# Kernel tuning notes

Hardware: AMD Instinct MI355X
Metric: run time of the kernel (lower is better)

Reference implementation:

```python
import jax, jax.numpy as jnp
import numpy as np

B, S, D = 2, 2048, 1024
H, HD = 16, 64  # num_heads, head_dim; H*HD == D


def setup_inputs() -> dict:
    key = jax.random.key(0)
    ks = jax.random.split(key, 5)
    scale = 1.0 / np.sqrt(D)
    return {
        "inputs": jax.random.normal(ks[0], (B, S, D), jnp.float32),
        "Wq": jax.random.normal(ks[1], (D, H * HD), jnp.float32) * scale,
        "bq": jnp.zeros((H * HD,), jnp.float32),
        "Wk": jax.random.normal(ks[2], (D, H * HD), jnp.float32) * scale,
        "bk": jnp.zeros((H * HD,), jnp.float32),
        "Wv": jax.random.normal(ks[3], (D, H * HD), jnp.float32) * scale,
        "bv": jnp.zeros((H * HD,), jnp.float32),
        "Wo": jax.random.normal(ks[4], (H * HD, D), jnp.float32) * scale,
        "bo": jnp.zeros((D,), jnp.float32),
    }


def reference(inputs, Wq, bq, Wk, bk, Wv, bv, Wo, bo):
    b, s, _ = inputs.shape
    # QKV projections, split into heads: [b, s, H, HD]
    q = (inputs @ Wq + bq).reshape(b, s, H, HD)
    k = (inputs @ Wk + bk).reshape(b, s, H, HD)
    v = (inputs @ Wv + bv).reshape(b, s, H, HD)
    # scaled dot-product attention (non-causal, full)
    scores = jnp.einsum('bqhd,bkhd->bhqk', q, k) / jnp.sqrt(jnp.float32(HD))
    attn = jax.nn.softmax(scores, axis=-1)
    out = jnp.einsum('bhql,blhd->bqhd', attn, v).reshape(b, s, H * HD)
    return out @ Wo + bo
```

## Files before the change

kernel.cpp:

```cpp
#include <hip/hip_runtime.h>
#include <hip/hip_bf16.h>

typedef __attribute__((ext_vector_type(8))) _Float16 half8;
typedef __attribute__((ext_vector_type(4))) _Float16 half4;
typedef __attribute__((ext_vector_type(2))) _Float16 half2v;
typedef __attribute__((ext_vector_type(4))) __fp16 fp16x4;
typedef __attribute__((ext_vector_type(4))) float f32x4;

#define MFMA16(a, b, c) __builtin_amdgcn_mfma_f32_16x16x32_f16(a, b, c, 0, 0, 0)
#define MFMA16K16(a, b, c)                                                         \
    __builtin_amdgcn_mfma_f32_16x16x16f16(__builtin_bit_cast(fp16x4, a),           \
                                          __builtin_bit_cast(fp16x4, b), c, 0, 0, 0)

typedef const __attribute__((address_space(1))) unsigned int GU32;
typedef __attribute__((address_space(3))) unsigned int LU32;

__device__ __forceinline__ void async_copy16(const _Float16* g, _Float16* l) {
    __builtin_amdgcn_global_load_lds((GU32*)g, (LU32*)l, 16, 0, 0);
}

__device__ __forceinline__ half2v pack2(float a, float b) {
    return __builtin_bit_cast(half2v, __builtin_amdgcn_cvt_pkrtz(a, b));
}

#define QSCALE 0.18033688011112042f

__global__ __launch_bounds__(256) void prep(
    const float* __restrict__ X, _Float16* __restrict__ Xh,
    const float* __restrict__ W0, const float* __restrict__ W1,
    const float* __restrict__ W2, const float* __restrict__ W3,
    _Float16* __restrict__ T0, _Float16* __restrict__ T1,
    _Float16* __restrict__ T2, _Float16* __restrict__ T3) {
    __shared__ float t[32][33];
    const int bid = blockIdx.x, tid = threadIdx.x;
    if (bid < 4096) {
        int i = (bid * 256 + tid) * 4;
        float4 v = *(const float4*)(X + i);
        half4 o = {(_Float16)v.x, (_Float16)v.y, (_Float16)v.z, (_Float16)v.w};
        *(half4*)(Xh + i) = o;
    } else {
        const int bid2 = bid - 4096;
        const int z = bid2 >> 10, tt = bid2 & 1023;
        const int bx = tt & 31, by = tt >> 5;
        const int tx = tid & 31, ty = tid >> 5;
        const float* src = z == 0 ? W0 : z == 1 ? W1 : z == 2 ? W2 : W3;
        _Float16* dst    = z == 0 ? T0 : z == 1 ? T1 : z == 2 ? T2 : T3;
        const int x = bx * 32 + tx;
        const int y0 = by * 32;
        for (int i = ty; i < 32; i += 8)
            t[i][tx] = src[(size_t)(y0 + i) * 1024 + x];
        __syncthreads();
        const int nx = y0 + tx;
        const int ny = bx * 32;
        for (int i = ty; i < 32; i += 8)
            dst[(size_t)(ny + i) * 1024 + nx] = (_Float16)t[tx][i];
    }
}

__global__ __launch_bounds__(256) void qkv_gemm(
    const _Float16* __restrict__ Xh,
    const _Float16* __restrict__ WTq, const _Float16* __restrict__ WTk,
    const _Float16* __restrict__ WTv,
    const float* __restrict__ bq, const float* __restrict__ bk,
    const float* __restrict__ bv,
    _Float16* __restrict__ Qo, _Float16* __restrict__ Ko,
    _Float16* __restrict__ Vto) {
    __shared__ __attribute__((aligned(16))) _Float16 Als[128 * 32];
    __shared__ __attribute__((aligned(16))) _Float16 Bls[128 * 32];

    const int wsel = blockIdx.y >> 3;
    const _Float16* WT = wsel == 0 ? WTq : wsel == 1 ? WTk : WTv;
    const float* bias  = wsel == 0 ? bq  : wsel == 1 ? bk  : bv;

    const int tid = threadIdx.x, w = tid >> 6, lane = tid & 63;
    const int quad = lane >> 4, l16 = lane & 15;
    const int wr = (w >> 1) * 64, wc = (w & 1) * 64;
    const int mBase = blockIdx.x * 128, nBase = (blockIdx.y & 7) * 128;
    const _Float16* Ab = Xh + (size_t)mBase * 1024;
    const _Float16* Bb = WT + (size_t)nBase * 1024;

    f32x4 acc[4][4] = {};

    for (int k0 = 0; k0 < 1024; k0 += 32) {
        __syncthreads();
#pragma unroll
        for (int iss = 0; iss < 2; ++iss) {
            int u = iss * 256 + tid;
            int r = u >> 2, c8 = (u & 3) * 8;
            _Float16* lA = Als + (size_t)(iss * 256 + (tid & 192)) * 8;
            _Float16* lB = Bls + (size_t)(iss * 256 + (tid & 192)) * 8;
            async_copy16(Ab + (size_t)r * 1024 + k0 + c8, lA);
            async_copy16(Bb + (size_t)r * 1024 + k0 + c8, lB);
        }
        __syncthreads();
        half8 af[4], bfr[4];
#pragma unroll
        for (int i = 0; i < 4; ++i) af[i]  = ((const half8*)Als)[(wr + i * 16 + l16) * 4 + quad];
#pragma unroll
        for (int j = 0; j < 4; ++j) bfr[j] = ((const half8*)Bls)[(wc + j * 16 + l16) * 4 + quad];
#pragma unroll
        for (int i = 0; i < 4; ++i)
#pragma unroll
            for (int j = 0; j < 4; ++j) acc[i][j] = MFMA16(af[i], bfr[j], acc[i][j]);
    }

    const float scale = (wsel == 0) ? QSCALE : 1.0f;
#pragma unroll
    for (int i = 0; i < 4; ++i) {
        const int row = mBase + wr + i * 16 + quad * 4;
#pragma unroll
        for (int j = 0; j < 4; ++j) {
            const int col = nBase + wc + j * 16 + l16;
            const float bb = bias[col];
            const int hh = col >> 6, hd = col & 63;
            if (wsel == 2) {
                const int bi = row >> 11, s = row & 2047;
                half4 pv;
#pragma unroll
                for (int r = 0; r < 4; ++r) pv[r] = (_Float16)((acc[i][j][r] + bb) * scale);
                *(half4*)(Vto + ((size_t)(bi * 16 + hh) * 64 + hd) * 2048 + s) = pv;
            } else {
                _Float16* dst = (wsel == 0) ? Qo : Ko;
#pragma unroll
                for (int r = 0; r < 4; ++r) {
                    const int token = row + r;
                    const int bi = token >> 11, s = token & 2047;
                    dst[((size_t)(bi * 16 + hh) * 2048 + s) * 64 + hd] =
                        (_Float16)((acc[i][j][r] + bb) * scale);
                }
            }
        }
    }
}

__global__ __launch_bounds__(512) void attn_kernel(
    const _Float16* __restrict__ Q, const _Float16* __restrict__ K,
    const _Float16* __restrict__ Vt, _Float16* __restrict__ O) {
    const int bh = blockIdx.y;
    const int b = bh >> 4, h = bh & 15;
    const int qt = blockIdx.x;
    const int tid = threadIdx.x, w = tid >> 6, lane = tid & 63;
    const int quad = lane >> 4, l16 = lane & 15;
    const int ws2 = w & 3, stream = w >> 2;

    __shared__ __attribute__((aligned(16))) _Float16 smem[32768];
    _Float16 (*Kls)[2][4096] = (_Float16(*)[2][4096])smem;
    _Float16 (*Vls)[2][4096] = (_Float16(*)[2][4096])(smem + 16384);

    const _Float16* Qb = Q  + (size_t)bh * 2048 * 64;
    const _Float16* Kb = K  + (size_t)bh * 2048 * 64;
    const _Float16* Vb = Vt + (size_t)bh * 64 * 2048;

    const int stid = tid & 255, sgrp = tid >> 8;
    const int u0 = stid, u1 = 256 + stid;
    const int r0 = u0 >> 3, c0 = (u0 & 7) ^ (r0 & 7);
    const int r1 = u1 >> 3, c1 = (u1 & 7) ^ (r1 & 7);
    const int lbase0 = (stid & 192) * 8;
    const int lbase1 = 2048 + (stid & 192) * 8;

    half8 qf[2][2];
#pragma unroll
    for (int g = 0; g < 2; ++g) {
        const int q = qt * 128 + ws2 * 32 + g * 16 + l16;
#pragma unroll
        for (int kc = 0; kc < 2; ++kc)
            qf[g][kc] = *(const half8*)(Qb + (size_t)q * 64 + kc * 32 + quad * 8);
    }

    f32x4 oacc[2][4] = {};
    float l[2] = {0.f, 0.f};

    {
        const int nb = sgrp * 64;
        _Float16* kd = &Kls[sgrp][0][0];
        _Float16* vd = &Vls[sgrp][0][0];
        async_copy16(Kb + (size_t)(nb + r0) * 64 + c0 * 8, kd + lbase0);
        async_copy16(Kb + (size_t)(nb + r1) * 64 + c1 * 8, kd + lbase1);
        async_copy16(Vb + (size_t)r0 * 2048 + nb + c0 * 8, vd + lbase0);
        async_copy16(Vb + (size_t)r1 * 2048 + nb + c1 * 8, vd + lbase1);
    }

    const int sw = l16 & 7;
    for (int it = 0; it < 16; ++it) {
        __syncthreads();
        const _Float16* Kc = &Kls[stream][it & 1][0];
        const _Float16* Vc = &Vls[stream][it & 1][0];
        if (it + 1 < 16) {
            const int nb = (2 * (it + 1) + sgrp) * 64;
            _Float16* kd = &Kls[sgrp][(it + 1) & 1][0];
            _Float16* vd = &Vls[sgrp][(it + 1) & 1][0];
            async_copy16(Kb + (size_t)(nb + r0) * 64 + c0 * 8, kd + lbase0);
            async_copy16(Kb + (size_t)(nb + r1) * 64 + c1 * 8, kd + lbase1);
            async_copy16(Vb + (size_t)r0 * 2048 + nb + c0 * 8, vd + lbase0);
            async_copy16(Vb + (size_t)r1 * 2048 + nb + c1 * 8, vd + lbase1);
        }
        f32x4 s0[4] = {}, s1[4] = {};
#pragma unroll
        for (int nt = 0; nt < 4; ++nt) {
            const int key = nt * 16 + l16;
            half8 k0 = *(const half8*)(Kc + ((size_t)key * 8 + (quad ^ sw)) * 8);
            half8 k1 = *(const half8*)(Kc + ((size_t)key * 8 + ((4 + quad) ^ sw)) * 8);
            s0[nt] = MFMA16(k0, qf[0][0], s0[nt]);
            s0[nt] = MFMA16(k1, qf[0][1], s0[nt]);
            s1[nt] = MFMA16(k0, qf[1][0], s1[nt]);
            s1[nt] = MFMA16(k1, qf[1][1], s1[nt]);
        }
        half4 pB[2][4];
#pragma unroll
        for (int g = 0; g < 2; ++g) {
            f32x4* s = g ? s1 : s0;
#pragma unroll
            for (int nt = 0; nt < 4; ++nt) {
                float p0 = __builtin_amdgcn_exp2f(s[nt][0]);
                float p1 = __builtin_amdgcn_exp2f(s[nt][1]);
                float p2 = __builtin_amdgcn_exp2f(s[nt][2]);
                float p3 = __builtin_amdgcn_exp2f(s[nt][3]);
                l[g] += (p0 + p1) + (p2 + p3);
                ((half2v*)&pB[g][nt])[0] = pack2(p0, p1);
                ((half2v*)&pB[g][nt])[1] = pack2(p2, p3);
            }
        }
#pragma unroll
        for (int nt = 0; nt < 4; ++nt) {
            const int chunk = (nt << 1) + (quad >> 1);
#pragma unroll
            for (int j = 0; j < 4; ++j) {
                const int hd = j * 16 + l16;
                half4 vf = *(const half4*)(Vc + ((size_t)hd * 8 + (chunk ^ sw)) * 8 +
                                           (quad & 1) * 4);
                oacc[0][j] = MFMA16K16(vf, pB[0][nt], oacc[0][j]);
                oacc[1][j] = MFMA16K16(vf, pB[1][nt], oacc[1][j]);
            }
        }
    }
    __syncthreads();
    float* red  = (float*)smem;
    float* redl = (float*)smem + 4 * 64 * 36;
    const int rb = (ws2 * 64 + lane) * 36;
    if (stream == 1) {
#pragma unroll
        for (int g = 0; g < 2; ++g) {
#pragma unroll
            for (int j = 0; j < 4; ++j)
                *(f32x4*)&red[rb + (g * 4 + j) * 4] = oacc[g][j];
            redl[(ws2 * 64 + lane) * 2 + g] = l[g];
        }
    }
    __syncthreads();
    if (stream == 0) {
#pragma unroll
        for (int g = 0; g < 2; ++g) {
#pragma unroll
            for (int j = 0; j < 4; ++j) {
                f32x4 o2 = *(const f32x4*)&red[rb + (g * 4 + j) * 4];
#pragma unroll
                for (int r = 0; r < 4; ++r) oacc[g][j][r] += o2[r];
            }
            float lt = l[g] + redl[(ws2 * 64 + lane) * 2 + g];
            lt += __shfl_xor(lt, 16);
            lt += __shfl_xor(lt, 32);
            const float inv = __builtin_amdgcn_rcpf(lt);
            const int token = b * 2048 + qt * 128 + ws2 * 32 + g * 16 + l16;
#pragma unroll
            for (int j = 0; j < 4; ++j) {
                half4 ov;
#pragma unroll
                for (int r = 0; r < 4; ++r) ov[r] = (_Float16)(oacc[g][j][r] * inv);
                *(half4*)&O[(size_t)token * 1024 + h * 64 + j * 16 + quad * 4] = ov;
            }
        }
    }
}

__global__ __launch_bounds__(256) void out_gemm(
    const _Float16* __restrict__ Oh, const _Float16* __restrict__ WTo,
    const float* __restrict__ bo, float* __restrict__ Y) {
    __shared__ __attribute__((aligned(16))) _Float16 Als[64 * 32];
    __shared__ __attribute__((aligned(16))) _Float16 Bls[128 * 32];
    const int tid = threadIdx.x, w = tid >> 6, lane = tid & 63;
    const int quad = lane >> 4, l16 = lane & 15;
    const int wr = (w >> 1) * 32, wc = (w & 1) * 64;
    const int mBase = blockIdx.x * 64, nBase = blockIdx.y * 128;
    const _Float16* Ab = Oh + (size_t)mBase * 1024;
    const _Float16* Bb = WTo + (size_t)nBase * 1024;

    f32x4 acc[2][4] = {};
    for (int k0 = 0; k0 < 1024; k0 += 32) {
        __syncthreads();
        {
            int r = tid >> 2, c8 = (tid & 3) * 8;
            _Float16* lA = Als + (size_t)(tid & 192) * 8;
            async_copy16(Ab + (size_t)r * 1024 + k0 + c8, lA);
        }
#pragma unroll
        for (int iss = 0; iss < 2; ++iss) {
            int u = iss * 256 + tid;
            int r = u >> 2, c8 = (u & 3) * 8;
            _Float16* lB = Bls + (size_t)(iss * 256 + (tid & 192)) * 8;
            async_copy16(Bb + (size_t)r * 1024 + k0 + c8, lB);
        }
        __syncthreads();
        half8 af[2], bfr[4];
#pragma unroll
        for (int i = 0; i < 2; ++i) af[i]  = ((const half8*)Als)[(wr + i * 16 + l16) * 4 + quad];
#pragma unroll
        for (int j = 0; j < 4; ++j) bfr[j] = ((const half8*)Bls)[(wc + j * 16 + l16) * 4 + quad];
#pragma unroll
        for (int i = 0; i < 2; ++i)
#pragma unroll
            for (int j = 0; j < 4; ++j) acc[i][j] = MFMA16(af[i], bfr[j], acc[i][j]);
    }
#pragma unroll
    for (int i = 0; i < 2; ++i) {
        const int row = mBase + wr + i * 16 + quad * 4;
#pragma unroll
        for (int j = 0; j < 4; ++j) {
            const int col = nBase + wc + j * 16 + l16;
            const float bb = bo[col];
#pragma unroll
            for (int r = 0; r < 4; ++r)
                Y[(size_t)(row + r) * 1024 + col] = acc[i][j][r] + bb;
        }
    }
}

extern "C" void kernel_launch(void* const* d_in, const int* in_sizes, int n_in,
                              void* d_out, int out_size, void* d_ws, size_t ws_size,
                              hipStream_t stream) {
    const float* X  = (const float*)d_in[0];
    const float* Wq = (const float*)d_in[1];
    const float* bq = (const float*)d_in[2];
    const float* Wk = (const float*)d_in[3];
    const float* bk = (const float*)d_in[4];
    const float* Wv = (const float*)d_in[5];
    const float* bv = (const float*)d_in[6];
    const float* Wo = (const float*)d_in[7];
    const float* bo = (const float*)d_in[8];
    float* Y = (float*)d_out;

    char* ws = (char*)d_ws;
    _Float16* Xh  = (_Float16*)(ws);
    _Float16* WTq = (_Float16*)(ws + (8ull << 20));
    _Float16* WTk = (_Float16*)(ws + (10ull << 20));
    _Float16* WTv = (_Float16*)(ws + (12ull << 20));
    _Float16* WTo = (_Float16*)(ws + (14ull << 20));
    _Float16* Qh  = (_Float16*)(ws + (16ull << 20));
    _Float16* Kh  = (_Float16*)(ws + (24ull << 20));
    _Float16* Vth = (_Float16*)(ws + (32ull << 20));
    _Float16* Oh  = (_Float16*)(ws + (40ull << 20));

    prep<<<8192, 256, 0, stream>>>(X, Xh, Wq, Wk, Wv, Wo, WTq, WTk, WTv, WTo);
    qkv_gemm<<<dim3(32, 24), 256, 0, stream>>>(Xh, WTq, WTk, WTv, bq, bk, bv, Qh, Kh, Vth);
    attn_kernel<<<dim3(16, 32), 512, 0, stream>>>(Qh, Kh, Vth, Oh);
    out_gemm<<<dim3(64, 8), 256, 0, stream>>>(Oh, WTo, bo, Y);
}
```

Measured before the change: 200.5 us.

## Swizzle GEMM LDS tiles and store Q/K token-major to simplify epilogue

Both projection GEMMs now XOR-swizzle the 16-byte chunk position within each LDS row, on the global load side and the fragment read side, to cut LDS bank conflicts on the MFMA operand reads. Q and K are also written token-major ([b, s, h*64]) with contiguous column stores instead of a per-head scattered layout. The attention kernel indexes Q and K with a 1024 stride to match. This trades a simpler, more coalesced QKV epilogue for strided 128-byte row reads of K and Q in attention.

```diff
diff --git a/kernel.cpp b/kernel.cpp
--- a/kernel.cpp
+++ b/kernel.cpp
@@ -24,6 +24,7 @@
 }
 
 #define QSCALE 0.18033688011112042f
+
 
 __global__ __launch_bounds__(256) void prep(
     const float* __restrict__ X, _Float16* __restrict__ Xh,
@@ -79,25 +80,35 @@
     const _Float16* Ab = Xh + (size_t)mBase * 1024;
     const _Float16* Bb = WT + (size_t)nBase * 1024;
 
+    const int sr0 = tid >> 2,          sc0 = (tid & 3) ^ ((sr0 >> 1) & 3);
+    const int sr1 = (256 + tid) >> 2,  sc1 = (tid & 3) ^ ((sr1 >> 1) & 3);
+
     f32x4 acc[4][4] = {};
 
     for (int k0 = 0; k0 < 1024; k0 += 32) {
         __syncthreads();
-#pragma unroll
-        for (int iss = 0; iss < 2; ++iss) {
-            int u = iss * 256 + tid;
-            int r = u >> 2, c8 = (u & 3) * 8;
-            _Float16* lA = Als + (size_t)(iss * 256 + (tid & 192)) * 8;
-            _Float16* lB = Bls + (size_t)(iss * 256 + (tid & 192)) * 8;
-            async_copy16(Ab + (size_t)r * 1024 + k0 + c8, lA);
-            async_copy16(Bb + (size_t)r * 1024 + k0 + c8, lB);
+        {
+            _Float16* lA0 = Als + (size_t)(tid & 192) * 8;
+            _Float16* lB0 = Bls + (size_t)(tid & 192) * 8;
+            _Float16* lA1 = Als + (size_t)(256 + (tid & 192)) * 8;
+            _Float16* lB1 = Bls + (size_t)(256 + (tid & 192)) * 8;
+            async_copy16(Ab + (size_t)sr0 * 1024 + k0 + sc0 * 8, lA0);
+            async_copy16(Bb + (size_t)sr0 * 1024 + k0 + sc0 * 8, lB0);
+            async_copy16(Ab + (size_t)sr1 * 1024 + k0 + sc1 * 8, lA1);
+            async_copy16(Bb + (size_t)sr1 * 1024 + k0 + sc1 * 8, lB1);
         }
         __syncthreads();
         half8 af[4], bfr[4];
 #pragma unroll
-        for (int i = 0; i < 4; ++i) af[i]  = ((const half8*)Als)[(wr + i * 16 + l16) * 4 + quad];
-#pragma unroll
-        for (int j = 0; j < 4; ++j) bfr[j] = ((const half8*)Bls)[(wc + j * 16 + l16) * 4 + quad];
+        for (int i = 0; i < 4; ++i) {
+            const int row = wr + i * 16 + l16;
+            af[i] = ((const half8*)Als)[row * 4 + (quad ^ ((row >> 1) & 3))];
+        }
+#pragma unroll
+        for (int j = 0; j < 4; ++j) {
+            const int row = wc + j * 16 + l16;
+            bfr[j] = ((const half8*)Bls)[row * 4 + (quad ^ ((row >> 1) & 3))];
+        }
 #pragma unroll
         for (int i = 0; i < 4; ++i)
 #pragma unroll
@@ -112,8 +123,8 @@
         for (int j = 0; j < 4; ++j) {
             const int col = nBase + wc + j * 16 + l16;
             const float bb = bias[col];
-            const int hh = col >> 6, hd = col & 63;
             if (wsel == 2) {
+                const int hh = col >> 6, hd = col & 63;
                 const int bi = row >> 11, s = row & 2047;
                 half4 pv;
 #pragma unroll
@@ -122,12 +133,9 @@
             } else {
                 _Float16* dst = (wsel == 0) ? Qo : Ko;
 #pragma unroll
-                for (int r = 0; r < 4; ++r) {
-                    const int token = row + r;
-                    const int bi = token >> 11, s = token & 2047;
-                    dst[((size_t)(bi * 16 + hh) * 2048 + s) * 64 + hd] =
+                for (int r = 0; r < 4; ++r)
+                    dst[(size_t)(row + r) * 1024 + col] =
                         (_Float16)((acc[i][j][r] + bb) * scale);
-                }
             }
         }
     }
@@ -141,14 +149,14 @@
     const int qt = blockIdx.x;
     const int tid = threadIdx.x, w = tid >> 6, lane = tid & 63;
     const int quad = lane >> 4, l16 = lane & 15;
-    const int ws2 = w & 3, stream = w >> 2;
+    const int ws2 = w & 3, kstream = w >> 2;
 
     __shared__ __attribute__((aligned(16))) _Float16 smem[32768];
     _Float16 (*Kls)[2][4096] = (_Float16(*)[2][4096])smem;
     _Float16 (*Vls)[2][4096] = (_Float16(*)[2][4096])(smem + 16384);
 
-    const _Float16* Qb = Q  + (size_t)bh * 2048 * 64;
-    const _Float16* Kb = K  + (size_t)bh * 2048 * 64;
+    const _Float16* Qb = Q  + (size_t)b * 2048 * 1024 + h * 64;
+    const _Float16* Kb = K  + (size_t)b * 2048 * 1024 + h * 64;
     const _Float16* Vb = Vt + (size_t)bh * 64 * 2048;
 
     const int stid = tid & 255, sgrp = tid >> 8;
@@ -164,7 +172,7 @@
         const int q = qt * 128 + ws2 * 32 + g * 16 + l16;
 #pragma unroll
         for (int kc = 0; kc < 2; ++kc)
-            qf[g][kc] = *(const half8*)(Qb + (size_t)q * 64 + kc * 32 + quad * 8);
+            qf[g][kc] = *(const half8*)(Qb + (size_t)q * 1024 + kc * 32 + quad * 8);
     }
 
     f32x4 oacc[2][4] = {};
@@ -174,8 +182,8 @@
         const int nb = sgrp * 64;
         _Float16* kd = &Kls[sgrp][0][0];
         _Float16* vd = &Vls[sgrp][0][0];
-        async_copy16(Kb + (size_t)(nb + r0) * 64 + c0 * 8, kd + lbase0);
-        async_copy16(Kb + (size_t)(nb + r1) * 64 + c1 * 8, kd + lbase1);
+        async_copy16(Kb + (size_t)(nb + r0) * 1024 + c0 * 8, kd + lbase0);
+        async_copy16(Kb + (size_t)(nb + r1) * 1024 + c1 * 8, kd + lbase1);
         async_copy16(Vb + (size_t)r0 * 2048 + nb + c0 * 8, vd + lbase0);
         async_copy16(Vb + (size_t)r1 * 2048 + nb + c1 * 8, vd + lbase1);
     }
@@ -183,14 +191,14 @@
     const int sw = l16 & 7;
     for (int it = 0; it < 16; ++it) {
         __syncthreads();
-        const _Float16* Kc = &Kls[stream][it & 1][0];
-        const _Float16* Vc = &Vls[stream][it & 1][0];
+        const _Float16* Kc = &Kls[kstream][it & 1][0];
+        const _Float16* Vc = &Vls[kstream][it & 1][0];
         if (it + 1 < 16) {
             const int nb = (2 * (it + 1) + sgrp) * 64;
             _Float16* kd = &Kls[sgrp][(it + 1) & 1][0];
             _Float16* vd = &Vls[sgrp][(it + 1) & 1][0];
-            async_copy16(Kb + (size_t)(nb + r0) * 64 + c0 * 8, kd + lbase0);
-            async_copy16(Kb + (size_t)(nb + r1) * 64 + c1 * 8, kd + lbase1);
+            async_copy16(Kb + (size_t)(nb + r0) * 1024 + c0 * 8, kd + lbase0);
+            async_copy16(Kb + (size_t)(nb + r1) * 1024 + c1 * 8, kd + lbase1);
             async_copy16(Vb + (size_t)r0 * 2048 + nb + c0 * 8, vd + lbase0);
             async_copy16(Vb + (size_t)r1 * 2048 + nb + c1 * 8, vd + lbase1);
         }
@@ -237,7 +245,7 @@
     float* red  = (float*)smem;
     float* redl = (float*)smem + 4 * 64 * 36;
     const int rb = (ws2 * 64 + lane) * 36;
-    if (stream == 1) {
+    if (kstream == 1) {
 #pragma unroll
         for (int g = 0; g < 2; ++g) {
 #pragma unroll
@@ -247,7 +255,7 @@
         }
     }
     __syncthreads();
-    if (stream == 0) {
+    if (kstream == 0) {
 #pragma unroll
         for (int g = 0; g < 2; ++g) {
 #pragma unroll
@@ -284,27 +292,32 @@
     const _Float16* Ab = Oh + (size_t)mBase * 1024;
     const _Float16* Bb = WTo + (size_t)nBase * 1024;
 
+    const int sr0 = tid >> 2,         sc0 = (tid & 3) ^ ((sr0 >> 1) & 3);
+    const int sr1 = (256 + tid) >> 2, sc1 = (tid & 3) ^ ((sr1 >> 1) & 3);
+
     f32x4 acc[2][4] = {};
     for (int k0 = 0; k0 < 1024; k0 += 32) {
         __syncthreads();
         {
-            int r = tid >> 2, c8 = (tid & 3) * 8;
-            _Float16* lA = Als + (size_t)(tid & 192) * 8;
-            async_copy16(Ab + (size_t)r * 1024 + k0 + c8, lA);
-        }
-#pragma unroll
-        for (int iss = 0; iss < 2; ++iss) {
-            int u = iss * 256 + tid;
-            int r = u >> 2, c8 = (u & 3) * 8;
-            _Float16* lB = Bls + (size_t)(iss * 256 + (tid & 192)) * 8;
-            async_copy16(Bb + (size_t)r * 1024 + k0 + c8, lB);
+            _Float16* lA0 = Als + (size_t)(tid & 192) * 8;
+            _Float16* lB0 = Bls + (size_t)(tid & 192) * 8;
+            _Float16* lB1 = Bls + (size_t)(256 + (tid & 192)) * 8;
+            async_copy16(Ab + (size_t)sr0 * 1024 + k0 + sc0 * 8, lA0);
+            async_copy16(Bb + (size_t)sr0 * 1024 + k0 + sc0 * 8, lB0);
+            async_copy16(Bb + (size_t)sr1 * 1024 + k0 + sc1 * 8, lB1);
         }
         __syncthreads();
         half8 af[2], bfr[4];
 #pragma unroll
-        for (int i = 0; i < 2; ++i) af[i]  = ((const half8*)Als)[(wr + i * 16 + l16) * 4 + quad];
-#pragma unroll
-        for (int j = 0; j < 4; ++j) bfr[j] = ((const half8*)Bls)[(wc + j * 16 + l16) * 4 + quad];
+        for (int i = 0; i < 2; ++i) {
+            const int row = wr + i * 16 + l16;
+            af[i] = ((const half8*)Als)[row * 4 + (quad ^ ((row >> 1) & 3))];
+        }
+#pragma unroll
+        for (int j = 0; j < 4; ++j) {
+            const int row = wc + j * 16 + l16;
+            bfr[j] = ((const half8*)Bls)[row * 4 + (quad ^ ((row >> 1) & 3))];
+        }
 #pragma unroll
         for (int i = 0; i < 2; ++i)
 #pragma unroll
```

Result: no change. 199.4 us (-0.5%).
